# Kernel optimization log

Hardware: AMD Instinct MI355X
Metric: run time of the kernel (lower is better)

The kernel has to match this reference:

```python
import jax, jax.numpy as jnp
import numpy as np

EMBED_DIM = 1024
NUM_HEADS = 16
HEAD_DIM = EMBED_DIM // NUM_HEADS
SCALE = HEAD_DIM ** -0.5


def setup_inputs() -> dict:
    key = jax.random.key(0)
    ks = jax.random.split(key, 11)
    B, SQ, SK = 4, 1024, 2048
    std = EMBED_DIM ** -0.5
    inp = {
        'query': jax.random.normal(ks[0], (B, SQ, EMBED_DIM), jnp.float32),
        'key': jax.random.normal(ks[1], (B, SK, EMBED_DIM), jnp.float32),
        'value': jax.random.normal(ks[2], (B, SK, EMBED_DIM), jnp.float32),
        'Wq': jax.random.normal(ks[3], (EMBED_DIM, EMBED_DIM), jnp.float32) * std,
        'bq': jnp.zeros((EMBED_DIM,), jnp.float32),
        'Wk': jax.random.normal(ks[4], (EMBED_DIM, EMBED_DIM), jnp.float32) * std,
        'bk': jnp.zeros((EMBED_DIM,), jnp.float32),
        'Wv': jax.random.normal(ks[5], (EMBED_DIM, EMBED_DIM), jnp.float32) * std,
        'bv': jnp.zeros((EMBED_DIM,), jnp.float32),
        'Wo': jax.random.normal(ks[6], (EMBED_DIM, EMBED_DIM), jnp.float32) * std,
        'bo': jnp.zeros((EMBED_DIM,), jnp.float32),
    }
    return inp


def reference(query, key, value, Wq, bq, Wk, bk, Wv, bv, Wo, bo):
    B, SQ, _ = query.shape
    SK = key.shape[1]
    # projections (torch Linear: x @ W^T + b)
    q = query @ Wq.T + bq
    k = key @ Wk.T + bk
    v = value @ Wv.T + bv
    # split heads -> [B, H, S, Dh]
    q = q.reshape(B, SQ, NUM_HEADS, HEAD_DIM).transpose(0, 2, 1, 3)
    k = k.reshape(B, SK, NUM_HEADS, HEAD_DIM).transpose(0, 2, 1, 3)
    v = v.reshape(B, SK, NUM_HEADS, HEAD_DIM).transpose(0, 2, 1, 3)
    scores = jnp.einsum('bhqd,bhkd->bhqk', q, k) * SCALE
    attn = jax.nn.softmax(scores, axis=-1)  # dropout p=0 -> identity
    attended = jnp.einsum('bhqk,bhkd->bhqd', attn, v)
    attended = attended.transpose(0, 2, 1, 3).reshape(B, SQ, EMBED_DIM)
    output = attended @ Wo.T + bo
    mean_attn = attn.mean(axis=1)  # average over heads -> [B, SQ, SK]
    return output, mean_attn
```

## Files before the change

kernel.cpp:

```cpp
#include <hip/hip_runtime.h>
#include <hip/hip_bf16.h>
#include <math.h>

#define EMBED 1024
#define NHEADS 16
#define HDIM 64
#define BATCH 4
#define SQL 1024
#define SKL 2048
#define PSC 0.18033688f

typedef unsigned short u16;
typedef __attribute__((ext_vector_type(4))) float f32x4;
typedef __attribute__((ext_vector_type(8))) __bf16 bf16x8;
typedef __attribute__((ext_vector_type(8))) short s16x8;
typedef __attribute__((ext_vector_type(4))) short s16x4;
typedef __attribute__((ext_vector_type(8))) u16 u16x8;
typedef __attribute__((ext_vector_type(2))) unsigned u32x2;

__device__ __forceinline__ u16 f2bf(float x) {
    __hip_bfloat16 h = __float2bfloat16(x);
    return *reinterpret_cast<u16*>(&h);
}
__device__ __forceinline__ float bf2f(u16 u) {
    __hip_bfloat16 h;
    *reinterpret_cast<u16*>(&h) = u;
    return __bfloat162float(h);
}
__device__ __forceinline__ unsigned permpack(float e0, float e1) {
    return __builtin_amdgcn_perm(__builtin_bit_cast(unsigned, e1),
                                 __builtin_bit_cast(unsigned, e0), 0x07060302u);
}
__device__ __forceinline__ f32x4 mfma16(s16x8 a, s16x8 b, f32x4 c) {
    return __builtin_amdgcn_mfma_f32_16x16x32_bf16(
        __builtin_bit_cast(bf16x8, a), __builtin_bit_cast(bf16x8, b), c, 0, 0, 0);
}
__device__ __forceinline__ f32x4 mfma16k16(s16x4 a, s16x4 b, f32x4 c) {
    return __builtin_amdgcn_mfma_f32_16x16x16bf16_1k(a, b, c, 0, 0, 0);
}
__device__ __forceinline__ void gload16(const void* g, void* l) {
    __builtin_amdgcn_global_load_lds(
        (const __attribute__((address_space(1))) void*)g,
        (__attribute__((address_space(3))) void*)l, 16, 0, 0);
}
__device__ __forceinline__ void stage8k(const char* g, size_t rstrideB,
                                        char* ldsPlane, int w, int lane) {
    int r = w * 8 + (lane >> 3);
    int cs = (lane & 7) ^ (r & 7);
    gload16(g + (size_t)r * rstrideB + cs * 16, ldsPlane + (size_t)w * 1024);
}
#define SBAR() { __builtin_amdgcn_sched_barrier(0); \
    __builtin_amdgcn_s_barrier(); __builtin_amdgcn_sched_barrier(0); }

__global__ __launch_bounds__(256)
void cvt_in(const float* __restrict__ Wq, const float* __restrict__ Wk,
            const float* __restrict__ Wv, const float* __restrict__ Wo,
            const float* __restrict__ query, const float* __restrict__ key,
            u16* __restrict__ Wqh, u16* __restrict__ Wkh,
            u16* __restrict__ Wvh, u16* __restrict__ Woh,
            u16* __restrict__ Qbf, u16* __restrict__ Kbf) {
    int bid = blockIdx.x;
    const float* src; u16* dh;
    if (bid < 512)        { src = Wq; dh = Wqh; }
    else if (bid < 1024)  { bid -= 512;  src = Wk; dh = Wkh; }
    else if (bid < 1536)  { bid -= 1024; src = Wv; dh = Wvh; }
    else if (bid < 2048)  { bid -= 1536; src = Wo; dh = Woh; }
    else if (bid < 4096)  { bid -= 2048; src = query; dh = Qbf; }
    else                  { bid -= 4096; src = key; dh = Kbf; }
    size_t i = ((size_t)bid * 256 + threadIdx.x) * 8;
    float4 a = *(const float4*)&src[i];
    float4 b = *(const float4*)&src[i + 4];
    float v[8] = {a.x, a.y, a.z, a.w, b.x, b.y, b.z, b.w};
    u16x8 hi;
#pragma unroll
    for (int j = 0; j < 8; ++j) hi[j] = f2bf(v[j]);
    *(u16x8*)&dh[i] = hi;
}

#define QK_LOAD(S, kk) { \
    au##S##0 = *(const u16x8*)&Af[(size_t)(rowBase + srow) * 1024 + (kk) + sc]; \
    au##S##1 = *(const u16x8*)&Af[(size_t)(rowBase + srow) * 1024 + (kk) + sc + 8]; \
    wh##S##0 = *(const u16x8*)&Wu[(size_t)(colBase + srow) * 1024 + (kk) + sc]; \
    wh##S##1 = *(const u16x8*)&Wu[(size_t)(colBase + srow) * 1024 + (kk) + sc + 8]; }

#define QK_WRITE(S) { \
    *(u16x8*)&sA[srow * 40 + sc] = au##S##0; \
    *(u16x8*)&sA[srow * 40 + sc + 8] = au##S##1; \
    *(u16x8*)&sB[srow * 40 + sc] = wh##S##0; \
    *(u16x8*)&sB[srow * 40 + sc + 8] = wh##S##1; }

#define GEMM_COMPUTE() { \
    s16x8 afh[4], bfh[4]; \
    _Pragma("unroll") for (int mi = 0; mi < 4; ++mi) { \
        int ai = (wm * 64 + mi * 16 + (lane & 15)) * 40 + (lane >> 4) * 8; \
        afh[mi] = *(const s16x8*)&sA[ai]; \
    } \
    _Pragma("unroll") for (int ni = 0; ni < 4; ++ni) { \
        int bi = (wn * 64 + ni * 16 + (lane & 15)) * 40 + (lane >> 4) * 8; \
        bfh[ni] = *(const s16x8*)&sB[bi]; \
    } \
    _Pragma("unroll") for (int mi = 0; mi < 4; ++mi) \
        _Pragma("unroll") for (int ni = 0; ni < 4; ++ni) \
            acc[mi][ni] = mfma16(afh[mi], bfh[ni], acc[mi][ni]); }

__global__ __launch_bounds__(256)
void gemm_qk(const u16* __restrict__ Qbf, const u16* __restrict__ Kbf,
             const u16* __restrict__ Wqh, const u16* __restrict__ Wkh,
             const float* __restrict__ bq, const float* __restrict__ bk,
             u16* __restrict__ Qhi, u16* __restrict__ Khi) {
    __shared__ u16 sA[128 * 40];
    __shared__ u16 sB[128 * 40];

    const int t = threadIdx.x;
    const int lane = t & 63;
    const int w = t >> 6;
    const int wm = w >> 1, wn = w & 1;
    const int srow = t >> 1;
    const int sc = (t & 1) * 16;

    const int bid = blockIdx.x;
    const int p = bid % 96;
    const int col = bid / 96;
    const int isK = p >= 32;
    const int rowBase = (isK ? p - 32 : p) * 128;
    const int colBase = col * 128;
    const u16* Af = isK ? Kbf : Qbf;
    const u16* Wu = isK ? Wkh : Wqh;
    const float* bias = isK ? bk : bq;
    const float scale = isK ? 1.0f : PSC;
    const int bshift = isK ? 11 : 10;
    u16* Yout = isK ? Khi : Qhi;

    f32x4 acc[4][4];
#pragma unroll
    for (int i = 0; i < 4; ++i)
#pragma unroll
        for (int j = 0; j < 4; ++j) acc[i][j] = (f32x4){0.f, 0.f, 0.f, 0.f};

    u16x8 au00, au01, au10, au11;
    u16x8 wh00, wh01, wh10, wh11;

    QK_LOAD(0, 0)
    QK_LOAD(1, 32)

    for (int k0 = 0; k0 < 1024; k0 += 64) {
        __syncthreads();
        QK_WRITE(0)
        __syncthreads();
        if (k0 + 64 < 1024) QK_LOAD(0, k0 + 64)
        GEMM_COMPUTE()
        __syncthreads();
        QK_WRITE(1)
        __syncthreads();
        if (k0 + 96 < 1024) QK_LOAD(1, k0 + 96)
        GEMM_COMPUTE()
    }

#pragma unroll
    for (int mi = 0; mi < 4; ++mi)
#pragma unroll
        for (int ni = 0; ni < 4; ++ni)
#pragma unroll
            for (int rr = 0; rr < 4; ++rr) {
                int mg = rowBase + wm * 64 + mi * 16 + (lane >> 4) * 4 + rr;
                int ng = colBase + wn * 64 + ni * 16 + (lane & 15);
                float y = (acc[mi][ni][rr] + bias[ng]) * scale;
                int bb = mg >> bshift, s = mg & ((1 << bshift) - 1);
                size_t idx = ((((size_t)(bb * 16 + (ng >> 6))) << bshift) + s) * 64 + (ng & 63);
                Yout[idx] = f2bf(y);
            }
}

__global__ __launch_bounds__(256)
void gemm_vproj(const u16* __restrict__ Au, const float* __restrict__ Wf,
                const float* __restrict__ bias, u16* __restrict__ VTh) {
    __shared__ u16 sA[128 * 40];
    __shared__ u16 sB[128 * 40];

    const int t = threadIdx.x;
    const int lane = t & 63;
    const int w = t >> 6;
    const int wm = w >> 1, wn = w & 1;
    const int rowBase = blockIdx.y * 128;
    const int colBase = blockIdx.x * 128;
    const int srow = t >> 1;
    const int sc = (t & 1) * 16;

    f32x4 acc[4][4];
#pragma unroll
    for (int i = 0; i < 4; ++i)
#pragma unroll
        for (int j = 0; j < 4; ++j) acc[i][j] = (f32x4){0.f, 0.f, 0.f, 0.f};

    u16x8 au00, au01, au10, au11;
    float bx0[16], bx1[16];

#define VP_LOAD(S, kk) { \
    au##S##0 = *(const u16x8*)&Au[(size_t)(rowBase + srow) * 1024 + (kk) + sc]; \
    au##S##1 = *(const u16x8*)&Au[(size_t)(rowBase + srow) * 1024 + (kk) + sc + 8]; \
    _Pragma("unroll") for (int j = 0; j < 4; ++j) \
        *(float4*)&bx##S[j * 4] = *(const float4*)&Wf[(size_t)(colBase + srow) * 1024 + (kk) + sc + j * 4]; }
#define VP_WRITE(S) { \
    *(u16x8*)&sA[srow * 40 + sc] = au##S##0; \
    *(u16x8*)&sA[srow * 40 + sc + 8] = au##S##1; \
    u16x8 b0, b1; \
    _Pragma("unroll") for (int j = 0; j < 8; ++j) { \
        b0[j] = f2bf(bx##S[j]); b1[j] = f2bf(bx##S[j + 8]); } \
    *(u16x8*)&sB[srow * 40 + sc] = b0; \
    *(u16x8*)&sB[srow * 40 + sc + 8] = b1; }

    VP_LOAD(0, 0)
    VP_LOAD(1, 32)

    for (int k0 = 0; k0 < 1024; k0 += 64) {
        __syncthreads();
        VP_WRITE(0)
        __syncthreads();
        if (k0 + 64 < 1024) VP_LOAD(0, k0 + 64)
        GEMM_COMPUTE()
        __syncthreads();
        VP_WRITE(1)
        __syncthreads();
        if (k0 + 96 < 1024) VP_LOAD(1, k0 + 96)
        GEMM_COMPUTE()
    }

#pragma unroll
    for (int mi = 0; mi < 4; ++mi)
#pragma unroll
        for (int ni = 0; ni < 4; ++ni)
#pragma unroll
            for (int rr = 0; rr < 4; ++rr) {
                int mg = rowBase + wm * 64 + mi * 16 + (lane >> 4) * 4 + rr;
                int ng = colBase + wn * 64 + ni * 16 + (lane & 15);
                float y = acc[mi][ni][rr] + bias[mg];
                size_t idx = ((size_t)((ng >> 11) * 16 + (mg >> 6)) * 64 + (mg & 63)) * 2048 + (ng & 2047);
                VTh[idx] = f2bf(y);
            }
}

__global__ __launch_bounds__(256)
void gemm_oproj(const u16* __restrict__ Au, const u16* __restrict__ Wu,
                const float* __restrict__ bias, float* __restrict__ Y0p) {
    __shared__ u16 sA[128 * 40];
    __shared__ u16 sB[128 * 40];

    const int t = threadIdx.x;
    const int lane = t & 63;
    const int w = t >> 6;
    const int wm = w >> 1, wn = w & 1;
    const int p = blockIdx.x % 32;
    const int rowBase = p * 128;
    const int colBase = (blockIdx.x / 32) * 128;
    const int srow = t >> 1;
    const int sc = (t & 1) * 16;

    f32x4 acc[4][4];
#pragma unroll
    for (int i = 0; i < 4; ++i)
#pragma unroll
        for (int j = 0; j < 4; ++j) acc[i][j] = (f32x4){0.f, 0.f, 0.f, 0.f};

    u16x8 au00, au01, au10, au11;
    u16x8 wh00, wh01, wh10, wh11;

#define OP_LOAD(S, kk) { \
    au##S##0 = *(const u16x8*)&Au[(size_t)(rowBase + srow) * 1024 + (kk) + sc]; \
    au##S##1 = *(const u16x8*)&Au[(size_t)(rowBase + srow) * 1024 + (kk) + sc + 8]; \
    wh##S##0 = *(const u16x8*)&Wu[(size_t)(colBase + srow) * 1024 + (kk) + sc]; \
    wh##S##1 = *(const u16x8*)&Wu[(size_t)(colBase + srow) * 1024 + (kk) + sc + 8]; }
#define OP_WRITE(S) { \
    *(u16x8*)&sA[srow * 40 + sc] = au##S##0; \
    *(u16x8*)&sA[srow * 40 + sc + 8] = au##S##1; \
    *(u16x8*)&sB[srow * 40 + sc] = wh##S##0; \
    *(u16x8*)&sB[srow * 40 + sc + 8] = wh##S##1; }

    OP_LOAD(0, 0)
    OP_LOAD(1, 32)

    for (int k0 = 0; k0 < 1024; k0 += 64) {
        __syncthreads();
        OP_WRITE(0)
        __syncthreads();
        if (k0 + 64 < 1024) OP_LOAD(0, k0 + 64)
        GEMM_COMPUTE()
        __syncthreads();
        OP_WRITE(1)
        __syncthreads();
        if (k0 + 96 < 1024) OP_LOAD(1, k0 + 96)
        GEMM_COMPUTE()
    }

#pragma unroll
    for (int mi = 0; mi < 4; ++mi)
#pragma unroll
        for (int ni = 0; ni < 4; ++ni)
#pragma unroll
            for (int rr = 0; rr < 4; ++rr) {
                int mg = rowBase + wm * 64 + mi * 16 + (lane >> 4) * 4 + rr;
                int ng = colBase + wn * 64 + ni * 16 + (lane & 15);
                Y0p[(size_t)mg * 1024 + ng] = acc[mi][ni][rr] + bias[ng];
            }
}

__global__ __launch_bounds__(512, 4)
void attn_O(const u16* __restrict__ Qhi, const u16* __restrict__ Khi,
            const u16* __restrict__ VT, u16* __restrict__ Att,
            float* __restrict__ llog) {
    __shared__ char lds[49152];
    float* sOf = (float*)lds;
    float* sL2t = (float*)(lds + 35840);
    float* sL2f = (float*)(lds + 36864);

    const int t = threadIdx.x;
    const int w = t >> 6, lane = t & 63;
    const int g = lane >> 4, c16 = lane & 15;
    const int qt = blockIdx.x >> 6;
    const int g6 = blockIdx.x & 63;
    const int b = g6 >> 4, h = g6 & 15;
    const int qbase = qt * 128;
    const int wq = w >> 1, wk = w & 1;
    const int kswz = (g ^ (c16 & 7)) << 4;
    const int vsw0 = (((wk * 4 + 0 + (g >> 1)) ^ (c16 & 7)) << 4) | ((g & 1) << 3);
    const int vsw1 = (((wk * 4 + 2 + (g >> 1)) ^ (c16 & 7)) << 4) | ((g & 1) << 3);

    const char* Kh_g = (const char*)(Khi + (size_t)(b * 16 + h) * SKL * 64);
    const char* V_g  = (const char*)(VT + (size_t)(b * 16 + h) * 64 * SKL);

    s16x8 qh[2][2];
    const size_t qrowbase = (size_t)(b * 16 + h) * SQL + qbase;
#pragma unroll
    for (int qf = 0; qf < 2; ++qf) {
        size_t qo = (qrowbase + wq * 32 + qf * 16 + c16) * 64 + g * 8;
        qh[qf][0] = *(const s16x8*)&Qhi[qo];
        qh[qf][1] = *(const s16x8*)&Qhi[qo + 32];
    }

    stage8k(Kh_g, 128, lds, w, lane);
    stage8k(V_g, 4096, lds + 24576, w, lane);
    stage8k(Kh_g + 8192, 128, lds + 8192, w, lane);
    stage8k(V_g + 128, 4096, lds + 24576 + 8192, w, lane);

    const s16x4 onesf = {(short)0x3F80, (short)0x3F80, (short)0x3F80, (short)0x3F80};
    f32x4 oacc[2][4];
    f32x4 lacc[2];
    float lsum[2] = {0.f, 0.f};
#pragma unroll
    for (int qf = 0; qf < 2; ++qf) {
        lacc[qf] = (f32x4){0.f, 0.f, 0.f, 0.f};
#pragma unroll
        for (int i = 0; i < 4; ++i) oacc[qf][i] = (f32x4){0.f, 0.f, 0.f, 0.f};
    }

    int cur = 0;
    for (int c = 0; c < 32; ++c) {
        if (c < 31) { asm volatile("s_waitcnt vmcnt(2)" ::: "memory"); }
        else        { asm volatile("s_waitcnt vmcnt(0)" ::: "memory"); }
        SBAR();
        if (c + 2 < 32) {
            int nb = cur + 2; if (nb >= 3) nb -= 3;
            stage8k(Kh_g + (size_t)(c + 2) * 8192, 128, lds + nb * 8192, w, lane);
            stage8k(V_g + (size_t)(c + 2) * 128, 4096, lds + 24576 + nb * 8192, w, lane);
        }
        char* curK = lds + cur * 8192;
        char* curV = lds + 24576 + cur * 8192;
#pragma unroll
        for (int kf = 0; kf < 2; ++kf) {
            int kb = (wk * 32 + kf * 16 + c16) * 128 + kswz;
            s16x8 kh0 = *(const s16x8*)(curK + kb);
            s16x8 kh1 = *(const s16x8*)(curK + (kb ^ 64));
            s16x4 pb[2];
#pragma unroll
            for (int qf = 0; qf < 2; ++qf) {
                f32x4 s = {0.f, 0.f, 0.f, 0.f};
                s = mfma16(kh0, qh[qf][0], s);
                s = mfma16(kh1, qh[qf][1], s);
                float e0 = exp2f(s[0]);
                float e1 = exp2f(s[1]);
                float e2 = exp2f(s[2]);
                float e3 = exp2f(s[3]);
                lsum[qf] += (e0 + e1) + (e2 + e3);
                u32x2 pu = {permpack(e0, e1), permpack(e2, e3)};
                pb[qf] = __builtin_bit_cast(s16x4, pu);
                lacc[qf] = mfma16k16(onesf, pb[qf], lacc[qf]);
            }
            int vs = kf ? vsw1 : vsw0;
#pragma unroll
            for (int df = 0; df < 4; ++df) {
                s16x4 vf = *(const s16x4*)(curV + (df * 16 + c16) * 128 + vs);
                oacc[0][df] = mfma16k16(vf, pb[0], oacc[0][df]);
                oacc[1][df] = mfma16k16(vf, pb[1], oacc[1][df]);
            }
        }
        ++cur; if (cur == 3) cur = 0;
    }

#pragma unroll
    for (int qf = 0; qf < 2; ++qf) {
        lsum[qf] += __shfl_xor(lsum[qf], 16, 64);
        lsum[qf] += __shfl_xor(lsum[qf], 32, 64);
    }
    __syncthreads();
#pragma unroll
    for (int qf = 0; qf < 2; ++qf)
        if (g == 0) {
            sL2t[wk * 128 + wq * 32 + qf * 16 + c16] = lacc[qf][0];
            sL2f[wk * 128 + wq * 32 + qf * 16 + c16] = lsum[qf];
        }

#pragma unroll
    for (int half = 0; half < 2; ++half) {
        if (half) __syncthreads();
        if ((wq >> 1) == half) {
            int qlocal = (wq & 1) * 32 + c16;
#pragma unroll
            for (int qf = 0; qf < 2; ++qf)
#pragma unroll
                for (int df = 0; df < 4; ++df)
#pragma unroll
                    for (int r = 0; r < 4; ++r)
                        sOf[wk * 4352 + (df * 16 + g * 4 + r) * 68 + qlocal + qf * 16] =
                            oacc[qf][df][r];
        }
        __syncthreads();
        {
            int q = t >> 3, dg = t & 7;
            float lt = sL2t[half * 64 + q] + sL2t[128 + half * 64 + q];
            float linv = 1.f / lt;
            u16x8 ov;
#pragma unroll
            for (int i = 0; i < 8; ++i) {
                int d = dg * 8 + i;
                ov[i] = f2bf((sOf[d * 68 + q] + sOf[4352 + d * 68 + q]) * linv);
            }
            *(u16x8*)&Att[(size_t)(b * SQL + qbase + half * 64 + q) * EMBED + h * 64 + dg * 8] = ov;
            if (dg == 0) {
                float lf = sL2f[half * 64 + q] + sL2f[128 + half * 64 + q];
                llog[(size_t)(b * 16 + h) * SQL + qbase + half * 64 + q] = log2f(lf);
            }
        }
    }
}

__global__ __launch_bounds__(512, 4)
void attn_mean(const u16* __restrict__ Qhi, const u16* __restrict__ Khi,
               const float* __restrict__ llog, float* __restrict__ meanOut) {
    __shared__ char lds[81920];

    const int t = threadIdx.x;
    const int w = t >> 6, lane = t & 63;
    const int g = lane >> 4, c16 = lane & 15;
    const int qt = blockIdx.x >> 6;
    const int low = blockIdx.x & 63;
    const int b = low >> 4, ks = low & 15;
    const int qbase = qt * 128;
    const int kbase = ks * 128;
    const int wq = w >> 1, wk = w & 1;
    const int kswz = (g ^ (c16 & 7)) << 4;

    const size_t QH_STRIDE = (size_t)SQL * 128;
    const size_t KH_STRIDE = (size_t)SKL * 128;
    const char* Qh_b = (const char*)(Qhi + ((size_t)(b * 16) * SQL + qbase) * 64);
    const char* Kh_b = (const char*)(Khi + ((size_t)(b * 16) * SKL + kbase) * 64);
    const float* ll_b = llog + (size_t)(b * 16) * SQL + qbase;

    f32x4 ma[2][4];
#pragma unroll
    for (int qf = 0; qf < 2; ++qf)
#pragma unroll
        for (int i = 0; i < 4; ++i) ma[qf][i] = (f32x4){0.f, 0.f, 0.f, 0.f};

    stage8k(Qh_b, 128, lds, w, lane);
    stage8k(Qh_b + 8192, 128, lds + 8192, w, lane);
    float lbA0 = ll_b[wq * 32 + c16];
    float lbA1 = ll_b[wq * 32 + 16 + c16];
    stage8k(Kh_b, 128, lds + 32768, w, lane);
    stage8k(Kh_b + 8192, 128, lds + 32768 + 8192, w, lane);
    stage8k(Qh_b + QH_STRIDE, 128, lds + 16384, w, lane);
    stage8k(Qh_b + QH_STRIDE + 8192, 128, lds + 16384 + 8192, w, lane);
    float lbB0 = ll_b[SQL + wq * 32 + c16];
    float lbB1 = ll_b[SQL + wq * 32 + 16 + c16];
    stage8k(Kh_b + KH_STRIDE, 128, lds + 32768 + 16384, w, lane);
    stage8k(Kh_b + KH_STRIDE + 8192, 128, lds + 32768 + 16384 + 8192, w, lane);

    int curK = 0;
    for (int h = 0; h < 16; ++h) {
        if (h < 15) { asm volatile("s_waitcnt vmcnt(4)" ::: "memory"); }
        else        { asm volatile("s_waitcnt vmcnt(0)" ::: "memory"); }
        SBAR();

        const char* sQ = lds + (h & 1) * 16384;
        s16x8 qa0, qa1, qc0, qc1;
        {
            int qb0 = (wq * 32 + c16) * 128 + kswz;
            qa0 = *(const s16x8*)(sQ + qb0);
            qa1 = *(const s16x8*)(sQ + (qb0 ^ 64));
            int qb1 = (wq * 32 + 16 + c16) * 128 + kswz;
            qc0 = *(const s16x8*)(sQ + qb1);
            qc1 = *(const s16x8*)(sQ + (qb1 ^ 64));
        }
        asm volatile("s_waitcnt lgkmcnt(0)" ::: "memory");
        SBAR();

        float lb0 = lbA0, lb1 = lbA1;
        lbA0 = lbB0; lbA1 = lbB1;

        if (h + 2 < 16) {
            const char* Qg = Qh_b + (size_t)(h + 2) * QH_STRIDE;
            char* qdst = lds + (h & 1) * 16384;
            stage8k(Qg, 128, qdst, w, lane);
            stage8k(Qg + 8192, 128, qdst + 8192, w, lane);
            lbB0 = ll_b[(size_t)(h + 2) * SQL + wq * 32 + c16];
            lbB1 = ll_b[(size_t)(h + 2) * SQL + wq * 32 + 16 + c16];
            const char* Kg = Kh_b + (size_t)(h + 2) * KH_STRIDE;
            int nb = curK + 2; if (nb >= 3) nb -= 3;
            char* kdst = lds + 32768 + nb * 16384;
            stage8k(Kg, 128, kdst, w, lane);
            stage8k(Kg + 8192, 128, kdst + 8192, w, lane);
        }

        const char* sK = lds + 32768 + curK * 16384;
#pragma unroll
        for (int kf = 0; kf < 4; ++kf) {
            int kb = (kf * 32 + wk * 16 + c16) * 128 + kswz;
            s16x8 kh0 = *(const s16x8*)(sK + kb);
            s16x8 kh1 = *(const s16x8*)(sK + (kb ^ 64));
            {
                f32x4 s = {0.f, 0.f, 0.f, 0.f};
                s = mfma16(kh0, qa0, s);
                s = mfma16(kh1, qa1, s);
                ma[0][kf][0] += exp2f(s[0] - lb0);
                ma[0][kf][1] += exp2f(s[1] - lb0);
                ma[0][kf][2] += exp2f(s[2] - lb0);
                ma[0][kf][3] += exp2f(s[3] - lb0);
            }
            {
                f32x4 s = {0.f, 0.f, 0.f, 0.f};
                s = mfma16(kh0, qc0, s);
                s = mfma16(kh1, qc1, s);
                ma[1][kf][0] += exp2f(s[0] - lb1);
                ma[1][kf][1] += exp2f(s[1] - lb1);
                ma[1][kf][2] += exp2f(s[2] - lb1);
                ma[1][kf][3] += exp2f(s[3] - lb1);
            }
        }
        ++curK; if (curK == 3) curK = 0;
    }

    const float s16c = 1.f / 16.f;
#pragma unroll
    for (int qf = 0; qf < 2; ++qf)
#pragma unroll
        for (int kf = 0; kf < 4; ++kf) {
            f32x4 m = ma[qf][kf];
            m[0] *= s16c; m[1] *= s16c; m[2] *= s16c; m[3] *= s16c;
            *(f32x4*)&meanOut[(size_t)(b * SQL + qbase + wq * 32 + qf * 16 + c16) * SKL +
                              kbase + kf * 32 + wk * 16 + g * 4] = m;
        }
}

extern "C" void kernel_launch(void* const* d_in, const int* in_sizes, int n_in,
                              void* d_out, int out_size, void* d_ws, size_t ws_size,
                              hipStream_t stream) {
    const float* query = (const float*)d_in[0];
    const float* key   = (const float*)d_in[1];
    const float* value = (const float*)d_in[2];
    const float* Wq = (const float*)d_in[3];
    const float* bq = (const float*)d_in[4];
    const float* Wk = (const float*)d_in[5];
    const float* bk = (const float*)d_in[6];
    const float* Wv = (const float*)d_in[7];
    const float* bv = (const float*)d_in[8];
    const float* Wo = (const float*)d_in[9];
    const float* bo = (const float*)d_in[10];

    float* out = (float*)d_out;
    float* meanOut = out + (size_t)BATCH * SQL * EMBED;

    u16* Qhi = (u16*)d_ws;
    u16* Khi = Qhi + (size_t)4096 * 1024;
    u16* VTh = Khi + (size_t)8192 * 1024;
    u16* Att = VTh + (size_t)8192 * 1024;
    float* llog = (float*)(Att + (size_t)4096 * 1024);
    u16* Wqh = (u16*)(llog + 64 * 1024);
    u16* Wkh = Wqh + (size_t)1024 * 1024;
    u16* Wvh = Wkh + (size_t)1024 * 1024;
    u16* Woh = Wvh + (size_t)1024 * 1024;
    u16* Qbf = Woh + (size_t)1024 * 1024;
    u16* Kbf = Qbf + (size_t)4096 * 1024;

    cvt_in<<<dim3(8192), 256, 0, stream>>>(Wq, Wk, Wv, Wo, query, key,
                                           Wqh, Wkh, Wvh, Woh, Qbf, Kbf);

    gemm_qk<<<dim3(768), 256, 0, stream>>>(Qbf, Kbf, Wqh, Wkh, bq, bk, Qhi, Khi);
    gemm_vproj<<<dim3(64, 8), 256, 0, stream>>>(Wvh, value, bv, VTh);

    attn_O<<<dim3(512), dim3(512), 0, stream>>>(Qhi, Khi, VTh, Att, llog);
    attn_mean<<<dim3(512), dim3(512), 0, stream>>>(Qhi, Khi, llog, meanOut);

    gemm_oproj<<<dim3(256), 256, 0, stream>>>(Att, Woh, bo, out);
}
```

Before: 209.7 us.

## Merge QK and V projection GEMMs; load Q from global in attn_mean

Value is now converted to bf16 in cvt_in, using the meanOut buffer as scratch, and the V projection joins the Q/K projection in a single gemm_qkv launch with role-dependent epilogues. This removes a separate launch and the in-loop fp32-to-bf16 conversion of the V operand. attn_mean stops staging Q through LDS: it loads Q fragments straight from global into registers in a two-head software pipeline and keeps only a three-slot K buffer in LDS, which shrinks shared memory use. The catch is that the meanOut scratch is only safe because attn_mean overwrites it later, and the branchy epilogue adds divergence-free but extra code per block.

```diff
diff --git a/kernel.cpp b/kernel.cpp
--- a/kernel.cpp
+++ b/kernel.cpp
@@ -56,9 +56,11 @@
 void cvt_in(const float* __restrict__ Wq, const float* __restrict__ Wk,
             const float* __restrict__ Wv, const float* __restrict__ Wo,
             const float* __restrict__ query, const float* __restrict__ key,
+            const float* __restrict__ value,
             u16* __restrict__ Wqh, u16* __restrict__ Wkh,
             u16* __restrict__ Wvh, u16* __restrict__ Woh,
-            u16* __restrict__ Qbf, u16* __restrict__ Kbf) {
+            u16* __restrict__ Qbf, u16* __restrict__ Kbf,
+            u16* __restrict__ Vbf) {
     int bid = blockIdx.x;
     const float* src; u16* dh;
     if (bid < 512)        { src = Wq; dh = Wqh; }
@@ -66,7 +68,8 @@
     else if (bid < 1536)  { bid -= 1024; src = Wv; dh = Wvh; }
     else if (bid < 2048)  { bid -= 1536; src = Wo; dh = Woh; }
     else if (bid < 4096)  { bid -= 2048; src = query; dh = Qbf; }
-    else                  { bid -= 4096; src = key; dh = Kbf; }
+    else if (bid < 8192)  { bid -= 4096; src = key; dh = Kbf; }
+    else                  { bid -= 8192; src = value; dh = Vbf; }
     size_t i = ((size_t)bid * 256 + threadIdx.x) * 8;
     float4 a = *(const float4*)&src[i];
     float4 b = *(const float4*)&src[i + 4];
@@ -104,10 +107,14 @@
             acc[mi][ni] = mfma16(afh[mi], bfh[ni], acc[mi][ni]); }
 
 __global__ __launch_bounds__(256)
-void gemm_qk(const u16* __restrict__ Qbf, const u16* __restrict__ Kbf,
-             const u16* __restrict__ Wqh, const u16* __restrict__ Wkh,
-             const float* __restrict__ bq, const float* __restrict__ bk,
-             u16* __restrict__ Qhi, u16* __restrict__ Khi) {
+void gemm_qkv(const u16* __restrict__ Qbf, const u16* __restrict__ Kbf,
+              const u16* __restrict__ Vbf,
+              const u16* __restrict__ Wqh, const u16* __restrict__ Wkh,
+              const u16* __restrict__ Wvh,
+              const float* __restrict__ bq, const float* __restrict__ bk,
+              const float* __restrict__ bv,
+              u16* __restrict__ Qhi, u16* __restrict__ Khi,
+              u16* __restrict__ VTh) {
     __shared__ u16 sA[128 * 40];
     __shared__ u16 sB[128 * 40];
 
@@ -119,17 +126,24 @@
     const int sc = (t & 1) * 16;
 
     const int bid = blockIdx.x;
-    const int p = bid % 96;
-    const int col = bid / 96;
-    const int isK = p >= 32;
-    const int rowBase = (isK ? p - 32 : p) * 128;
-    const int colBase = col * 128;
-    const u16* Af = isK ? Kbf : Qbf;
-    const u16* Wu = isK ? Wkh : Wqh;
-    const float* bias = isK ? bk : bq;
-    const float scale = isK ? 1.0f : PSC;
-    const int bshift = isK ? 11 : 10;
-    u16* Yout = isK ? Khi : Qhi;
+    int role, rowBase, colBase;
+    const u16 *Af, *Wu;
+    if (bid < 768) {
+        int p = bid % 96, col = bid / 96;
+        int isK = p >= 32;
+        role = isK ? 1 : 0;
+        rowBase = (isK ? p - 32 : p) * 128;
+        colBase = col * 128;
+        Af = isK ? Kbf : Qbf;
+        Wu = isK ? Wkh : Wqh;
+    } else {
+        int r = bid - 768;
+        role = 2;
+        rowBase = (r / 64) * 128;
+        colBase = (r % 64) * 128;
+        Af = Wvh;
+        Wu = Vbf;
+    }
 
     f32x4 acc[4][4];
 #pragma unroll
@@ -164,78 +178,22 @@
             for (int rr = 0; rr < 4; ++rr) {
                 int mg = rowBase + wm * 64 + mi * 16 + (lane >> 4) * 4 + rr;
                 int ng = colBase + wn * 64 + ni * 16 + (lane & 15);
-                float y = (acc[mi][ni][rr] + bias[ng]) * scale;
-                int bb = mg >> bshift, s = mg & ((1 << bshift) - 1);
-                size_t idx = ((((size_t)(bb * 16 + (ng >> 6))) << bshift) + s) * 64 + (ng & 63);
-                Yout[idx] = f2bf(y);
-            }
-}
-
-__global__ __launch_bounds__(256)
-void gemm_vproj(const u16* __restrict__ Au, const float* __restrict__ Wf,
-                const float* __restrict__ bias, u16* __restrict__ VTh) {
-    __shared__ u16 sA[128 * 40];
-    __shared__ u16 sB[128 * 40];
-
-    const int t = threadIdx.x;
-    const int lane = t & 63;
-    const int w = t >> 6;
-    const int wm = w >> 1, wn = w & 1;
-    const int rowBase = blockIdx.y * 128;
-    const int colBase = blockIdx.x * 128;
-    const int srow = t >> 1;
-    const int sc = (t & 1) * 16;
-
-    f32x4 acc[4][4];
-#pragma unroll
-    for (int i = 0; i < 4; ++i)
-#pragma unroll
-        for (int j = 0; j < 4; ++j) acc[i][j] = (f32x4){0.f, 0.f, 0.f, 0.f};
-
-    u16x8 au00, au01, au10, au11;
-    float bx0[16], bx1[16];
-
-#define VP_LOAD(S, kk) { \
-    au##S##0 = *(const u16x8*)&Au[(size_t)(rowBase + srow) * 1024 + (kk) + sc]; \
-    au##S##1 = *(const u16x8*)&Au[(size_t)(rowBase + srow) * 1024 + (kk) + sc + 8]; \
-    _Pragma("unroll") for (int j = 0; j < 4; ++j) \
-        *(float4*)&bx##S[j * 4] = *(const float4*)&Wf[(size_t)(colBase + srow) * 1024 + (kk) + sc + j * 4]; }
-#define VP_WRITE(S) { \
-    *(u16x8*)&sA[srow * 40 + sc] = au##S##0; \
-    *(u16x8*)&sA[srow * 40 + sc + 8] = au##S##1; \
-    u16x8 b0, b1; \
-    _Pragma("unroll") for (int j = 0; j < 8; ++j) { \
-        b0[j] = f2bf(bx##S[j]); b1[j] = f2bf(bx##S[j + 8]); } \
-    *(u16x8*)&sB[srow * 40 + sc] = b0; \
-    *(u16x8*)&sB[srow * 40 + sc + 8] = b1; }
-
-    VP_LOAD(0, 0)
-    VP_LOAD(1, 32)
-
-    for (int k0 = 0; k0 < 1024; k0 += 64) {
-        __syncthreads();
-        VP_WRITE(0)
-        __syncthreads();
-        if (k0 + 64 < 1024) VP_LOAD(0, k0 + 64)
-        GEMM_COMPUTE()
-        __syncthreads();
-        VP_WRITE(1)
-        __syncthreads();
-        if (k0 + 96 < 1024) VP_LOAD(1, k0 + 96)
-        GEMM_COMPUTE()
-    }
-
-#pragma unroll
-    for (int mi = 0; mi < 4; ++mi)
-#pragma unroll
-        for (int ni = 0; ni < 4; ++ni)
-#pragma unroll
-            for (int rr = 0; rr < 4; ++rr) {
-                int mg = rowBase + wm * 64 + mi * 16 + (lane >> 4) * 4 + rr;
-                int ng = colBase + wn * 64 + ni * 16 + (lane & 15);
-                float y = acc[mi][ni][rr] + bias[mg];
-                size_t idx = ((size_t)((ng >> 11) * 16 + (mg >> 6)) * 64 + (mg & 63)) * 2048 + (ng & 2047);
-                VTh[idx] = f2bf(y);
+                float y = acc[mi][ni][rr];
+                if (role == 2) {
+                    y += bv[mg];
+                    size_t idx = ((size_t)((ng >> 11) * 16 + (mg >> 6)) * 64 + (mg & 63)) * 2048 + (ng & 2047);
+                    VTh[idx] = f2bf(y);
+                } else if (role == 0) {
+                    y = (y + bq[ng]) * PSC;
+                    int bb = mg >> 10, s = mg & 1023;
+                    size_t idx = ((((size_t)(bb * 16 + (ng >> 6))) << 10) + s) * 64 + (ng & 63);
+                    Qhi[idx] = f2bf(y);
+                } else {
+                    y += bk[ng];
+                    int bb = mg >> 11, s = mg & 2047;
+                    size_t idx = ((((size_t)(bb * 16 + (ng >> 6))) << 11) + s) * 64 + (ng & 63);
+                    Khi[idx] = f2bf(y);
+                }
             }
 }
 
@@ -442,10 +400,49 @@
     }
 }
 
+#define MGROUP(S, hh) { \
+    const char* Kg = Kh_b + (size_t)(hh) * KH_STRIDE; \
+    char* kdst = lds + ((hh) % 3) * 16384; \
+    stage8k(Kg, 128, kdst, w, lane); \
+    stage8k(Kg + 8192, 128, kdst + 8192, w, lane); \
+    size_t qo = ((size_t)(b * 16 + (hh)) * SQL + qbase + wq * 32 + c16) * 64 + g * 8; \
+    qa##S##0 = *(const s16x8*)&Qhi[qo]; \
+    qa##S##1 = *(const s16x8*)&Qhi[qo + 32]; \
+    qc##S##0 = *(const s16x8*)&Qhi[qo + 1024]; \
+    qc##S##1 = *(const s16x8*)&Qhi[qo + 1024 + 32]; \
+    lb##S##0 = ll_b[(size_t)(hh) * SQL + wq * 32 + c16]; \
+    lb##S##1 = ll_b[(size_t)(hh) * SQL + wq * 32 + 16 + c16]; }
+
+#define MCOMP(S, hh) { \
+    const char* sK = lds + ((hh) % 3) * 16384; \
+    _Pragma("unroll") for (int kf = 0; kf < 4; ++kf) { \
+        int kb = (kf * 32 + wk * 16 + c16) * 128 + kswz; \
+        s16x8 kh0 = *(const s16x8*)(sK + kb); \
+        s16x8 kh1 = *(const s16x8*)(sK + (kb ^ 64)); \
+        { \
+            f32x4 s = {0.f, 0.f, 0.f, 0.f}; \
+            s = mfma16(kh0, qa##S##0, s); \
+            s = mfma16(kh1, qa##S##1, s); \
+            ma[0][kf][0] += exp2f(s[0] - lb##S##0); \
+            ma[0][kf][1] += exp2f(s[1] - lb##S##0); \
+            ma[0][kf][2] += exp2f(s[2] - lb##S##0); \
+            ma[0][kf][3] += exp2f(s[3] - lb##S##0); \
+        } \
+        { \
+            f32x4 s = {0.f, 0.f, 0.f, 0.f}; \
+            s = mfma16(kh0, qc##S##0, s); \
+            s = mfma16(kh1, qc##S##1, s); \
+            ma[1][kf][0] += exp2f(s[0] - lb##S##1); \
+            ma[1][kf][1] += exp2f(s[1] - lb##S##1); \
+            ma[1][kf][2] += exp2f(s[2] - lb##S##1); \
+            ma[1][kf][3] += exp2f(s[3] - lb##S##1); \
+        } \
+    } }
+
 __global__ __launch_bounds__(512, 4)
 void attn_mean(const u16* __restrict__ Qhi, const u16* __restrict__ Khi,
                const float* __restrict__ llog, float* __restrict__ meanOut) {
-    __shared__ char lds[81920];
+    __shared__ char lds[49152];
 
     const int t = threadIdx.x;
     const int w = t >> 6, lane = t & 63;
@@ -458,9 +455,7 @@
     const int wq = w >> 1, wk = w & 1;
     const int kswz = (g ^ (c16 & 7)) << 4;
 
-    const size_t QH_STRIDE = (size_t)SQL * 128;
     const size_t KH_STRIDE = (size_t)SKL * 128;
-    const char* Qh_b = (const char*)(Qhi + ((size_t)(b * 16) * SQL + qbase) * 64);
     const char* Kh_b = (const char*)(Khi + ((size_t)(b * 16) * SKL + kbase) * 64);
     const float* ll_b = llog + (size_t)(b * 16) * SQL + qbase;
 
@@ -470,81 +465,23 @@
 #pragma unroll
         for (int i = 0; i < 4; ++i) ma[qf][i] = (f32x4){0.f, 0.f, 0.f, 0.f};
 
-    stage8k(Qh_b, 128, lds, w, lane);
-    stage8k(Qh_b + 8192, 128, lds + 8192, w, lane);
-    float lbA0 = ll_b[wq * 32 + c16];
-    float lbA1 = ll_b[wq * 32 + 16 + c16];
-    stage8k(Kh_b, 128, lds + 32768, w, lane);
-    stage8k(Kh_b + 8192, 128, lds + 32768 + 8192, w, lane);
-    stage8k(Qh_b + QH_STRIDE, 128, lds + 16384, w, lane);
-    stage8k(Qh_b + QH_STRIDE + 8192, 128, lds + 16384 + 8192, w, lane);
-    float lbB0 = ll_b[SQL + wq * 32 + c16];
-    float lbB1 = ll_b[SQL + wq * 32 + 16 + c16];
-    stage8k(Kh_b + KH_STRIDE, 128, lds + 32768 + 16384, w, lane);
-    stage8k(Kh_b + KH_STRIDE + 8192, 128, lds + 32768 + 16384 + 8192, w, lane);
-
-    int curK = 0;
-    for (int h = 0; h < 16; ++h) {
-        if (h < 15) { asm volatile("s_waitcnt vmcnt(4)" ::: "memory"); }
-        else        { asm volatile("s_waitcnt vmcnt(0)" ::: "memory"); }
+    s16x8 qaA0, qaA1, qcA0, qcA1;
+    s16x8 qaB0, qaB1, qcB0, qcB1;
+    float lbA0, lbA1, lbB0, lbB1;
+
+    MGROUP(A, 0)
+    MGROUP(B, 1)
+
+    for (int hp = 0; hp < 16; hp += 2) {
+        asm volatile("s_waitcnt vmcnt(8)" ::: "memory");
         SBAR();
-
-        const char* sQ = lds + (h & 1) * 16384;
-        s16x8 qa0, qa1, qc0, qc1;
-        {
-            int qb0 = (wq * 32 + c16) * 128 + kswz;
-            qa0 = *(const s16x8*)(sQ + qb0);
-            qa1 = *(const s16x8*)(sQ + (qb0 ^ 64));
-            int qb1 = (wq * 32 + 16 + c16) * 128 + kswz;
-            qc0 = *(const s16x8*)(sQ + qb1);
-            qc1 = *(const s16x8*)(sQ + (qb1 ^ 64));
-        }
-        asm volatile("s_waitcnt lgkmcnt(0)" ::: "memory");
+        MCOMP(A, hp)
+        if (hp + 2 < 16) MGROUP(A, hp + 2)
+        if (hp + 3 < 16) { asm volatile("s_waitcnt vmcnt(8)" ::: "memory"); }
+        else             { asm volatile("s_waitcnt vmcnt(0)" ::: "memory"); }
         SBAR();
-
-        float lb0 = lbA0, lb1 = lbA1;
-        lbA0 = lbB0; lbA1 = lbB1;
-
-        if (h + 2 < 16) {
-            const char* Qg = Qh_b + (size_t)(h + 2) * QH_STRIDE;
-            char* qdst = lds + (h & 1) * 16384;
-            stage8k(Qg, 128, qdst, w, lane);
-            stage8k(Qg + 8192, 128, qdst + 8192, w, lane);
-            lbB0 = ll_b[(size_t)(h + 2) * SQL + wq * 32 + c16];
-            lbB1 = ll_b[(size_t)(h + 2) * SQL + wq * 32 + 16 + c16];
-            const char* Kg = Kh_b + (size_t)(h + 2) * KH_STRIDE;
-            int nb = curK + 2; if (nb >= 3) nb -= 3;
-            char* kdst = lds + 32768 + nb * 16384;
-            stage8k(Kg, 128, kdst, w, lane);
-            stage8k(Kg + 8192, 128, kdst + 8192, w, lane);
-        }
-
-        const char* sK = lds + 32768 + curK * 16384;
-#pragma unroll
-        for (int kf = 0; kf < 4; ++kf) {
-            int kb = (kf * 32 + wk * 16 + c16) * 128 + kswz;
-            s16x8 kh0 = *(const s16x8*)(sK + kb);
-            s16x8 kh1 = *(const s16x8*)(sK + (kb ^ 64));
-            {
-                f32x4 s = {0.f, 0.f, 0.f, 0.f};
-                s = mfma16(kh0, qa0, s);
-                s = mfma16(kh1, qa1, s);
-                ma[0][kf][0] += exp2f(s[0] - lb0);
-                ma[0][kf][1] += exp2f(s[1] - lb0);
-                ma[0][kf][2] += exp2f(s[2] - lb0);
-                ma[0][kf][3] += exp2f(s[3] - lb0);
-            }
-            {
-                f32x4 s = {0.f, 0.f, 0.f, 0.f};
-                s = mfma16(kh0, qc0, s);
-                s = mfma16(kh1, qc1, s);
-                ma[1][kf][0] += exp2f(s[0] - lb1);
-                ma[1][kf][1] += exp2f(s[1] - lb1);
-                ma[1][kf][2] += exp2f(s[2] - lb1);
-                ma[1][kf][3] += exp2f(s[3] - lb1);
-            }
-        }
-        ++curK; if (curK == 3) curK = 0;
+        MCOMP(B, hp + 1)
+        if (hp + 3 < 16) MGROUP(B, hp + 3)
     }
 
     const float s16c = 1.f / 16.f;
@@ -588,12 +525,13 @@
     u16* Woh = Wvh + (size_t)1024 * 1024;
     u16* Qbf = Woh + (size_t)1024 * 1024;
     u16* Kbf = Qbf + (size_t)4096 * 1024;
-
-    cvt_in<<<dim3(8192), 256, 0, stream>>>(Wq, Wk, Wv, Wo, query, key,
-                                           Wqh, Wkh, Wvh, Woh, Qbf, Kbf);
-
-    gemm_qk<<<dim3(768), 256, 0, stream>>>(Qbf, Kbf, Wqh, Wkh, bq, bk, Qhi, Khi);
-    gemm_vproj<<<dim3(64, 8), 256, 0, stream>>>(Wvh, value, bv, VTh);
+    u16* Vbf = (u16*)meanOut;
+
+    cvt_in<<<dim3(12288), 256, 0, stream>>>(Wq, Wk, Wv, Wo, query, key, value,
+                                            Wqh, Wkh, Wvh, Woh, Qbf, Kbf, Vbf);
+
+    gemm_qkv<<<dim3(1280), 256, 0, stream>>>(Qbf, Kbf, Vbf, Wqh, Wkh, Wvh,
+                                             bq, bk, bv, Qhi, Khi, VTh);
 
     attn_O<<<dim3(512), dim3(512), 0, stream>>>(Qhi, Khi, VTh, Att, llog);
     attn_mean<<<dim3(512), dim3(512), 0, stream>>>(Qhi, Khi, llog, meanOut);
```

New measurement: 325.4 us. +55.1%, slower.
